# Kernel optimization log

Hardware: AMD Instinct MI355X
Metric: run time of the kernel (lower is better)

Reference implementation:

```python
import jax, jax.numpy as jnp
import numpy as np

B, C_IN, N_IN, N_OUT = 4, 64, 8192, 8192
D1, F, H = 4, 15, 16384  # d+1, filter_size, max_hash_cnt
C_MID, C_OUT = 64, 64
LEAK = 0.01


def setup_inputs() -> dict:
    key = jax.random.key(0)
    ks = jax.random.split(key, 10)
    features = jax.random.normal(ks[0], (B, C_IN, N_IN), jnp.float32)
    in_barycentric = jax.random.uniform(ks[1], (B, D1, N_IN), dtype=jnp.float32)
    # global flat lattice offsets: local vertex id in [0,H) plus per-batch base b*(H+1)
    local_off = jax.random.randint(ks[2], (B, D1, N_IN), 0, H)
    base = (jnp.arange(B, dtype=jnp.int64) * (H + 1))[:, None, None]
    in_lattice_offset = local_off.astype(jnp.int64) + base
    # neighbor ids in [-1, H); -1 means missing -> maps to zero padding slot after +1
    blur_neighbors = (jax.random.randint(ks[3], (B, F, H), 0, H + 1) - 1).astype(jnp.int64)
    out_barycentric = jax.random.uniform(ks[4], (B, D1, N_OUT), dtype=jnp.float32)
    out_lattice_offset = jax.random.randint(ks[5], (B, D1, N_OUT), 0, H).astype(jnp.int64)
    # blur conv params: layer0 Conv2d(C_IN,C_MID,(F,1)) + LeakyReLU, layer1 Conv2d(C_MID,C_OUT,(1,1)) no relu
    W0 = jax.random.normal(ks[6], (C_MID, C_IN, F), jnp.float32) * 0.05
    b0 = jax.random.normal(ks[7], (C_MID,), jnp.float32) * 0.01
    W1 = jax.random.normal(ks[8], (C_OUT, C_MID), jnp.float32) * 0.1
    b1 = jax.random.normal(ks[9], (C_OUT,), jnp.float32) * 0.01
    bias = jnp.zeros((C_OUT,), jnp.float32)  # slice bias, initialized to zeros as in module
    return dict(features=features, in_barycentric=in_barycentric,
                in_lattice_offset=in_lattice_offset, blur_neighbors=blur_neighbors,
                out_barycentric=out_barycentric, out_lattice_offset=out_lattice_offset,
                W0=W0, b0=b0, W1=W1, b1=b1, bias=bias)


def reference(features, in_barycentric, in_lattice_offset, blur_neighbors,
              out_barycentric, out_lattice_offset, W0, b0, W1, b1, bias):
    b_sz, c_in, n_in = features.shape
    max_hash = blur_neighbors.shape[-1]
    # ---- splat: scatter-sum barycentric-weighted features onto lattice vertices ----
    vals = in_barycentric[:, None, :, :] * features[:, :, None, :]      # (B,C,d1,N)
    vals = vals.transpose(0, 2, 3, 1).reshape(-1, c_in)                  # (B*d1*N, C)
    idx = (in_lattice_offset + 1).reshape(-1)                            # (B*d1*N,)
    splat = jax.ops.segment_sum(vals, idx, num_segments=b_sz * (max_hash + 1))
    splat = splat.reshape(b_sz, max_hash + 1, c_in).transpose(0, 2, 1)   # (B,C,H+1)
    # normalization: splat of all-ones feature
    one_splat = jax.ops.segment_sum(in_barycentric.reshape(-1), idx,
                                    num_segments=b_sz * (max_hash + 1))
    one_splat = one_splat.reshape(b_sz, max_hash + 1)
    splat = splat / (one_splat + 1e-5)[:, None, :]
    # ---- blur: gather F neighbors per vertex, then conv over the filter axis ----
    spread = jax.vmap(lambda s, n: s[:, n])(splat, blur_neighbors + 1)   # (B,C,F,H)
    h0 = jnp.einsum('bcfh,ocf->boh', spread, W0) + b0[None, :, None]     # (B,C_mid,H)
    h0 = jnp.where(h0 > 0, h0, LEAK * h0)                                # LeakyReLU
    feat_blurred = jnp.einsum('boh,po->bph', h0, W1) + b1[None, :, None] # (B,C_out,H)
    # ---- slice: barycentric-weighted gather back to output points ----
    tmp = jax.vmap(lambda f, o: f[:, o])(feat_blurred, out_lattice_offset)  # (B,C_out,d1,N_out)
    sliced = (out_barycentric[:, None, :, :] * tmp).sum(axis=2)
    sliced = sliced + bias[None, :, None]
    return sliced
```

## Files before the change

### kernel.cpp

```cpp
#include <hip/hip_runtime.h>

#define NB 4
#define C_IN 64
#define N_IN 8192
#define N_OUT 8192
#define D1 4
#define FS 15
#define HSZ 16384
#define LEAK 0.01f
#define CAP 24
#define POISON 0xAAAAAAAAu

#define NVERT (NB*(HSZ+1))

typedef __attribute__((ext_vector_type(8))) short short8;
typedef __attribute__((ext_vector_type(4))) float floatx4;

#define SPLATB_OFF 0
#define SPLATB_FL  (NVERT*32)
#define W0B_OFF    (SPLATB_OFF + SPLATB_FL)
#define W0B_FL     (64*64*FS/2)
#define W1B_OFF    (W0B_OFF + W0B_FL)
#define W1B_FL     (64*64/2)
#define CNT_OFF    (W1B_OFF + W1B_FL)
#define CNT_FL     (NVERT)
#define BREG_OFF   (CNT_OFF + CNT_FL)
#define FEATB_OFF  (BREG_OFF)
#define FEATB_FL   (NB*N_IN*32)
#define ENTP_OFF   (FEATB_OFF + FEATB_FL)
#define ENTP_FL    (NVERT*CAP*2)
#define FB_OFF     (BREG_OFF)

__device__ inline ushort f2bf(float x) {
    uint u = __float_as_uint(x);
    return (ushort)((u + 0x7FFF + ((u >> 16) & 1)) >> 16);
}
__device__ inline float bf2f(ushort b) {
    return __uint_as_float(((uint)b) << 16);
}

__global__ __launch_bounds__(256) void prep(const float* __restrict__ feat,
                                            const float* __restrict__ W0,
                                            const float* __restrict__ W1,
                                            const int* __restrict__ off,
                                            const float* __restrict__ bary,
                                            ushort* __restrict__ featB,
                                            ushort* __restrict__ W0f,
                                            ushort* __restrict__ W1f,
                                            uint* __restrict__ cnt,
                                            int2* __restrict__ entp) {
    __shared__ float t[64 * 65];
    const int blk = blockIdx.x;
    const int tid = threadIdx.x;
    if (blk < 512) {
        const int b  = blk >> 7;
        const int nb = (blk & 127) << 6;
        const int l  = tid & 63;
        const int g  = tid >> 6;
#pragma unroll
        for (int i = 0; i < 16; ++i) {
            int c = g * 16 + i;
            t[c * 65 + l] = feat[((size_t)(b * 64 + c)) * N_IN + nb + l];
        }
        __syncthreads();
#pragma unroll
        for (int i = 0; i < 16; ++i) {
            int n = g * 16 + i;
            featB[((size_t)(b * N_IN) + nb + n) * 64 + l] = f2bf(t[l * 65 + n]);
        }
    } else if (blk < 1024) {
        int e = (blk - 512) * 256 + tid;
        int v = off[e] + 1;
        int n = e & (N_IN - 1);
        int b = e >> 15;
        uint old  = atomicAdd(&cnt[v], 1u);
        uint slot = (old >= POISON) ? (old - POISON) : old;
        if (slot < CAP) {
            int2 pr;
            pr.x = b * N_IN + n;
            pr.y = __float_as_int(bary[e]);
            entp[v * CAP + slot] = pr;
        }
    } else {
        int e = (blk - 1024) * 256 + tid;
        if (e < 64 * 64 * FS) {
            int j    = e & 7;
            int lane = (e >> 3) & 63;
            int ch   = (e >> 9) & 1;
            int ot   = (e >> 10) & 3;
            int f    = e >> 12;
            int o = ot * 16 + (lane & 15);
            int c = ch * 32 + ((lane >> 4) & 3) * 8 + j;
            W0f[e] = f2bf(W0[(o * 64 + c) * FS + f]);
        } else {
            int e2   = e - 64 * 64 * FS;
            int j    = e2 & 7;
            int lane = (e2 >> 3) & 63;
            int ch   = (e2 >> 9) & 1;
            int pt   = (e2 >> 10) & 3;
            int p = pt * 16 + (lane & 15);
            int o = ch * 32 + ((lane >> 4) & 3) * 8 + j;
            W1f[e2] = f2bf(W1[p * 64 + o]);
        }
    }
}

__global__ __launch_bounds__(256) void gather_splat(const ushort* __restrict__ featB,
                                                    uint* __restrict__ cnt,
                                                    const int2* __restrict__ entp,
                                                    ushort* __restrict__ splatB) {
    const int v    = blockIdx.x * 4 + (threadIdx.x >> 6);
    const int lane = threadIdx.x & 63;
    const int base = v * CAP;

    uint cv = cnt[v];
    int2 p0[4];
#pragma unroll
    for (int k = 0; k < 4; ++k)
        p0[k] = entp[base + k];
    if (lane == 0) cnt[v] = 0u;

    int c = (int)((cv >= POISON) ? (cv - POISON) : cv);
    if (c > CAP) c = CAP;

    float acc = 0.f, sw = 0.f;
    {
        const int kn = c;
        float fv[4];
#pragma unroll
        for (int k = 0; k < 4; ++k)
            fv[k] = bf2f(featB[(size_t)(p0[k].x & (NB * N_IN - 1)) * 64 + lane]);
#pragma unroll
        for (int k = 0; k < 4; ++k)
            if (k < kn) {
                float w = __int_as_float(p0[k].y);
                acc += w * fv[k]; sw += w;
            }
    }
    for (int e0 = 4; e0 < c; e0 += 4) {
        const int kn = c - e0;
        int2 p[4];
#pragma unroll
        for (int k = 0; k < 4; ++k)
            p[k] = entp[base + e0 + k];
        float fv[4];
#pragma unroll
        for (int k = 0; k < 4; ++k)
            if (k < kn) fv[k] = bf2f(featB[(size_t)(p[k].x & (NB * N_IN - 1)) * 64 + lane]);
#pragma unroll
        for (int k = 0; k < 4; ++k)
            if (k < kn) {
                float w = __int_as_float(p[k].y);
                acc += w * fv[k]; sw += w;
            }
    }
    splatB[(size_t)v * 64 + lane] = f2bf(acc / (sw + 1e-5f));
}

#define XSTR 72
__global__ __launch_bounds__(256, 4) void blur_mfma(const ushort* __restrict__ splatB,
                                                    const int* __restrict__ nbr,
                                                    const ushort* __restrict__ W0f,
                                                    const ushort* __restrict__ W1f,
                                                    const float* __restrict__ b0,
                                                    const float* __restrict__ b1,
                                                    ushort* __restrict__ fb) {
    __shared__ ushort Xs[2][64 * XSTR];

    const int tid = threadIdx.x;
    const int p   = blockIdx.x;
    const int b   = p & 3;
    const int hb  = (p >> 2) << 6;

    const int lane = tid & 63;
    const int w    = tid >> 6;
    const int ow   = w & 1;
    const int hw   = w >> 1;
    const int m    = lane & 15;
    const int q    = lane >> 4;

    const int r    = tid >> 2;
    const int sseg = (tid & 3) << 4;

    const int* nbase = nbr + (b * FS) * HSZ + hb;
    const size_t sbase = (size_t)b * (HSZ + 1) * 64;

    short8 acur[2][2], anxt[2][2];
#pragma unroll
    for (int ot = 0; ot < 2; ++ot)
#pragma unroll
        for (int ch = 0; ch < 2; ++ch)
            acur[ot][ch] = *(const short8*)&W0f[(((ow * 2 + ot) * 2 + ch) * 64 + lane) * 8];

    {
        int v = nbase[r] + 1;
        const ushort* row = splatB + sbase + (size_t)v * 64 + sseg;
        *(short8*)&Xs[0][r * XSTR + sseg]     = *(const short8*)&row[0];
        *(short8*)&Xs[0][r * XSTR + sseg + 8] = *(const short8*)&row[8];
    }
    int nv = nbase[HSZ + r] + 1;
    __syncthreads();

    floatx4 acc[2][2] = {};

    for (int f = 0; f < FS; ++f) {
        const int cur = f & 1, nxt = cur ^ 1;
        short8 px0, px1;
        int nn = 0;
        if (f < FS - 1) {
            const ushort* row = splatB + sbase + (size_t)nv * 64 + sseg;
            px0 = *(const short8*)&row[0];
            px1 = *(const short8*)&row[8];
#pragma unroll
            for (int ot = 0; ot < 2; ++ot)
#pragma unroll
                for (int ch = 0; ch < 2; ++ch)
                    anxt[ot][ch] = *(const short8*)
                        &W0f[((((f + 1) * 4 + ow * 2 + ot) * 2 + ch) * 64 + lane) * 8];
            if (f < FS - 2) nn = nbase[(f + 2) * HSZ + r] + 1;
        }
#pragma unroll
        for (int ch = 0; ch < 2; ++ch) {
            const int ko = ch * 32 + q * 8;
#pragma unroll
            for (int ht = 0; ht < 2; ++ht) {
                short8 bb = *(const short8*)&Xs[cur][(hw * 32 + ht * 16 + m) * XSTR + ko];
                acc[0][ht] = __builtin_amdgcn_mfma_f32_16x16x32_bf16(acur[0][ch], bb, acc[0][ht], 0, 0, 0);
                acc[1][ht] = __builtin_amdgcn_mfma_f32_16x16x32_bf16(acur[1][ch], bb, acc[1][ht], 0, 0, 0);
            }
        }
        if (f < FS - 1) {
            *(short8*)&Xs[nxt][r * XSTR + sseg]     = px0;
            *(short8*)&Xs[nxt][r * XSTR + sseg + 8] = px1;
            nv = nn;
#pragma unroll
            for (int ot = 0; ot < 2; ++ot)
#pragma unroll
                for (int ch = 0; ch < 2; ++ch)
                    acur[ot][ch] = anxt[ot][ch];
        }
        __syncthreads();
    }

    short8 a2[2][2];
#pragma unroll
    for (int pt = 0; pt < 2; ++pt)
#pragma unroll
        for (int ch = 0; ch < 2; ++ch)
            a2[pt][ch] = *(const short8*)&W1f[(((ow * 2 + pt) * 2 + ch) * 64 + lane) * 8];

    ushort* Hs = &Xs[0][0];
#pragma unroll
    for (int ot = 0; ot < 2; ++ot) {
        const float4 b0v = *(const float4*)(b0 + ow * 32 + ot * 16 + q * 4);
#pragma unroll
        for (int ht = 0; ht < 2; ++ht) {
            float v0 = acc[ot][ht][0] + b0v.x; v0 = v0 > 0.f ? v0 : LEAK * v0;
            float v1 = acc[ot][ht][1] + b0v.y; v1 = v1 > 0.f ? v1 : LEAK * v1;
            float v2 = acc[ot][ht][2] + b0v.z; v2 = v2 > 0.f ? v2 : LEAK * v2;
            float v3 = acc[ot][ht][3] + b0v.w; v3 = v3 > 0.f ? v3 : LEAK * v3;
            ushort4 hv;
            hv.x = f2bf(v0); hv.y = f2bf(v1); hv.z = f2bf(v2); hv.w = f2bf(v3);
            *(ushort4*)&Hs[(hw * 32 + ht * 16 + m) * XSTR + ow * 32 + ot * 16 + q * 4] = hv;
        }
    }
    __syncthreads();

    floatx4 acc2[2][2] = {};
#pragma unroll
    for (int ch = 0; ch < 2; ++ch) {
        const int ko = ch * 32 + q * 8;
#pragma unroll
        for (int ht = 0; ht < 2; ++ht) {
            short8 b2 = *(const short8*)&Hs[(hw * 32 + ht * 16 + m) * XSTR + ko];
            acc2[0][ht] = __builtin_amdgcn_mfma_f32_16x16x32_bf16(a2[0][ch], b2, acc2[0][ht], 0, 0, 0);
            acc2[1][ht] = __builtin_amdgcn_mfma_f32_16x16x32_bf16(a2[1][ch], b2, acc2[1][ht], 0, 0, 0);
        }
    }

#pragma unroll
    for (int pt = 0; pt < 2; ++pt) {
        const float4 b1v = *(const float4*)(b1 + ow * 32 + pt * 16 + q * 4);
#pragma unroll
        for (int ht = 0; ht < 2; ++ht) {
            ushort4 ov;
            ov.x = f2bf(acc2[pt][ht][0] + b1v.x);
            ov.y = f2bf(acc2[pt][ht][1] + b1v.y);
            ov.z = f2bf(acc2[pt][ht][2] + b1v.z);
            ov.w = f2bf(acc2[pt][ht][3] + b1v.w);
            *(ushort4*)&fb[((size_t)(b * HSZ) + hb + hw * 32 + ht * 16 + m) * 64
                           + ow * 32 + pt * 16 + q * 4] = ov;
        }
    }
}

__global__ __launch_bounds__(256) void slice_kernel(const ushort* __restrict__ fb,
                                                    const float* __restrict__ ob,
                                                    const int* __restrict__ off,
                                                    const float* __restrict__ bias,
                                                    float* __restrict__ out) {
    __shared__ float tile[64 * 17];
    const int blk  = blockIdx.x;
    const int b    = blk & 3;
    const int nb   = (blk >> 2) << 4;
    const int lane = threadIdx.x & 63;
    const int w    = threadIdx.x >> 6;

    const float bs = bias[lane];
#pragma unroll
    for (int t = 0; t < 4; ++t) {
        int nl = w * 4 + t;
        int n  = nb + nl;
        float acc = bs;
#pragma unroll
        for (int j = 0; j < D1; ++j) {
            float wj = ob[(b * D1 + j) * N_OUT + n];
            int   oj = off[(b * D1 + j) * N_OUT + n];
            acc += wj * bf2f(fb[((size_t)b * HSZ + oj) * 64 + lane]);
        }
        tile[lane * 17 + nl] = acc;
    }
    __syncthreads();
    {
        const int p  = threadIdx.x >> 2;
        const int c4 = (threadIdx.x & 3) << 2;
        float4 v;
        v.x = tile[p * 17 + c4 + 0];
        v.y = tile[p * 17 + c4 + 1];
        v.z = tile[p * 17 + c4 + 2];
        v.w = tile[p * 17 + c4 + 3];
        *(float4*)&out[((size_t)(b * 64 + p)) * N_OUT + nb + c4] = v;
    }
}

extern "C" void kernel_launch(void* const* d_in, const int* in_sizes, int n_in,
                              void* d_out, int out_size, void* d_ws, size_t ws_size,
                              hipStream_t stream) {
    const float* features = (const float*)d_in[0];
    const float* in_bary  = (const float*)d_in[1];
    const int*   in_off   = (const int*)d_in[2];
    const int*   nbr      = (const int*)d_in[3];
    const float* out_bary = (const float*)d_in[4];
    const int*   out_off  = (const int*)d_in[5];
    const float* W0       = (const float*)d_in[6];
    const float* b0       = (const float*)d_in[7];
    const float* W1       = (const float*)d_in[8];
    const float* b1       = (const float*)d_in[9];
    const float* bias     = (const float*)d_in[10];

    float*  ws     = (float*)d_ws;
    ushort* splatB = (ushort*)(ws + SPLATB_OFF);
    ushort* W0f    = (ushort*)(ws + W0B_OFF);
    ushort* W1f    = (ushort*)(ws + W1B_OFF);
    uint*   cnt    = (uint*)(ws + CNT_OFF);
    ushort* featB  = (ushort*)(ws + FEATB_OFF);
    int2*   entp   = (int2*)(ws + ENTP_OFF);
    ushort* fb     = (ushort*)(ws + FB_OFF);


    prep<<<1280, 256, 0, stream>>>(features, W0, W1, in_off, in_bary,
                                   featB, W0f, W1f, cnt, entp);
    gather_splat<<<NVERT / 4, 256, 0, stream>>>(featB, cnt, entp, splatB);
    blur_mfma<<<NB * (HSZ / 64), 256, 0, stream>>>(splatB, nbr, W0f, W1f, b0, b1, fb);
    slice_kernel<<<NB * (N_OUT / 16), 256, 0, stream>>>(fb, out_bary, out_off, bias, (float*)d_out);
}
```

Baseline: 131.5 us.

## Load blur gather operands directly into MFMA registers, drop LDS staging

The blur kernel now has each lane gather its own neighbor rows from global memory straight into MFMA B-operand registers, instead of staging them through a double-buffered shared-memory tile. This removes the per-filter-tap LDS writes, reads and __syncthreads barriers, and shrinks shared memory to the single H tile. In exchange each row is fetched redundantly by the two output-channel warps (ow=0/1), so global and L2 gather traffic roughly doubles and more registers are needed.

```diff
diff --git a/kernel.cpp b/kernel.cpp
--- a/kernel.cpp
+++ b/kernel.cpp
@@ -165,7 +165,7 @@
                                                     const float* __restrict__ b0,
                                                     const float* __restrict__ b1,
                                                     ushort* __restrict__ fb) {
-    __shared__ ushort Xs[2][64 * XSTR];
+    __shared__ ushort Hs[64 * XSTR];
 
     const int tid = threadIdx.x;
     const int p   = blockIdx.x;
@@ -179,11 +179,12 @@
     const int m    = lane & 15;
     const int q    = lane >> 4;
 
-    const int r    = tid >> 2;
-    const int sseg = (tid & 3) << 4;
-
     const int* nbase = nbr + (b * FS) * HSZ + hb;
-    const size_t sbase = (size_t)b * (HSZ + 1) * 64;
+    const ushort* sb = splatB + (size_t)b * (HSZ + 1) * 64;
+
+    const int h0  = hw * 32 + m;
+    const int h1  = h0 + 16;
+    const int koq = q * 8;
 
     short8 acur[2][2], anxt[2][2];
 #pragma unroll
@@ -192,54 +193,62 @@
         for (int ch = 0; ch < 2; ++ch)
             acur[ot][ch] = *(const short8*)&W0f[(((ow * 2 + ot) * 2 + ch) * 64 + lane) * 8];
 
+    int iv0 = nbase[h0] + 1;
+    int iv1 = nbase[h1] + 1;
+    short8 bcur[2][2], bnxt[2][2];
     {
-        int v = nbase[r] + 1;
-        const ushort* row = splatB + sbase + (size_t)v * 64 + sseg;
-        *(short8*)&Xs[0][r * XSTR + sseg]     = *(const short8*)&row[0];
-        *(short8*)&Xs[0][r * XSTR + sseg + 8] = *(const short8*)&row[8];
-    }
-    int nv = nbase[HSZ + r] + 1;
-    __syncthreads();
+        const ushort* r0 = sb + (size_t)iv0 * 64;
+        const ushort* r1 = sb + (size_t)iv1 * 64;
+        bcur[0][0] = *(const short8*)&r0[koq];
+        bcur[1][0] = *(const short8*)&r0[32 + koq];
+        bcur[0][1] = *(const short8*)&r1[koq];
+        bcur[1][1] = *(const short8*)&r1[32 + koq];
+    }
+    int nv0 = nbase[HSZ + h0] + 1;
+    int nv1 = nbase[HSZ + h1] + 1;
 
     floatx4 acc[2][2] = {};
 
     for (int f = 0; f < FS; ++f) {
-        const int cur = f & 1, nxt = cur ^ 1;
-        short8 px0, px1;
-        int nn = 0;
+        int nn0 = 0, nn1 = 0;
         if (f < FS - 1) {
-            const ushort* row = splatB + sbase + (size_t)nv * 64 + sseg;
-            px0 = *(const short8*)&row[0];
-            px1 = *(const short8*)&row[8];
+            const ushort* r0 = sb + (size_t)nv0 * 64;
+            const ushort* r1 = sb + (size_t)nv1 * 64;
+            bnxt[0][0] = *(const short8*)&r0[koq];
+            bnxt[1][0] = *(const short8*)&r0[32 + koq];
+            bnxt[0][1] = *(const short8*)&r1[koq];
+            bnxt[1][1] = *(const short8*)&r1[32 + koq];
 #pragma unroll
             for (int ot = 0; ot < 2; ++ot)
 #pragma unroll
                 for (int ch = 0; ch < 2; ++ch)
                     anxt[ot][ch] = *(const short8*)
                         &W0f[((((f + 1) * 4 + ow * 2 + ot) * 2 + ch) * 64 + lane) * 8];
-            if (f < FS - 2) nn = nbase[(f + 2) * HSZ + r] + 1;
-        }
-#pragma unroll
-        for (int ch = 0; ch < 2; ++ch) {
-            const int ko = ch * 32 + q * 8;
+            if (f < FS - 2) {
+                nn0 = nbase[(f + 2) * HSZ + h0] + 1;
+                nn1 = nbase[(f + 2) * HSZ + h1] + 1;
+            }
+        }
+#pragma unroll
+        for (int ch = 0; ch < 2; ++ch)
 #pragma unroll
             for (int ht = 0; ht < 2; ++ht) {
-                short8 bb = *(const short8*)&Xs[cur][(hw * 32 + ht * 16 + m) * XSTR + ko];
-                acc[0][ht] = __builtin_amdgcn_mfma_f32_16x16x32_bf16(acur[0][ch], bb, acc[0][ht], 0, 0, 0);
-                acc[1][ht] = __builtin_amdgcn_mfma_f32_16x16x32_bf16(acur[1][ch], bb, acc[1][ht], 0, 0, 0);
+                acc[0][ht] = __builtin_amdgcn_mfma_f32_16x16x32_bf16(acur[0][ch], bcur[ch][ht], acc[0][ht], 0, 0, 0);
+                acc[1][ht] = __builtin_amdgcn_mfma_f32_16x16x32_bf16(acur[1][ch], bcur[ch][ht], acc[1][ht], 0, 0, 0);
             }
-        }
         if (f < FS - 1) {
-            *(short8*)&Xs[nxt][r * XSTR + sseg]     = px0;
-            *(short8*)&Xs[nxt][r * XSTR + sseg + 8] = px1;
-            nv = nn;
+#pragma unroll
+            for (int ch = 0; ch < 2; ++ch)
+#pragma unroll
+                for (int ht = 0; ht < 2; ++ht)
+                    bcur[ch][ht] = bnxt[ch][ht];
 #pragma unroll
             for (int ot = 0; ot < 2; ++ot)
 #pragma unroll
                 for (int ch = 0; ch < 2; ++ch)
                     acur[ot][ch] = anxt[ot][ch];
-        }
-        __syncthreads();
+            nv0 = nn0; nv1 = nn1;
+        }
     }
 
     short8 a2[2][2];
@@ -249,7 +258,6 @@
         for (int ch = 0; ch < 2; ++ch)
             a2[pt][ch] = *(const short8*)&W1f[(((ow * 2 + pt) * 2 + ch) * 64 + lane) * 8];
 
-    ushort* Hs = &Xs[0][0];
 #pragma unroll
     for (int ot = 0; ot < 2; ++ot) {
         const float4 b0v = *(const float4*)(b0 + ow * 32 + ot * 16 + q * 4);
```

After: 151.1 us. 1.15x slower.

## Deepen blur gather pipeline to four LDS buffers, two filter taps per barrier

Applied to the files above, without the earlier changes.

The blur kernel's LDS staging grows from a double buffer to a four-slot ring. Each loop round now gathers two neighbor rows ahead and runs the MFMAs for two filter taps, which halves the number of __syncthreads and gives the global gathers more time to complete. W0 fragments are now loaded in the same round they are used instead of being prefetched one tap ahead. In exchange, LDS per block doubles, which may reduce occupancy, and register pressure rises because two gathered rows are held at once.

```diff
diff --git a/kernel.cpp b/kernel.cpp
--- a/kernel.cpp
+++ b/kernel.cpp
@@ -165,7 +165,7 @@
                                                     const float* __restrict__ b0,
                                                     const float* __restrict__ b1,
                                                     ushort* __restrict__ fb) {
-    __shared__ ushort Xs[2][64 * XSTR];
+    __shared__ ushort Xs[4][64 * XSTR];
 
     const int tid = threadIdx.x;
     const int p   = blockIdx.x;
@@ -185,61 +185,95 @@
     const int* nbase = nbr + (b * FS) * HSZ + hb;
     const size_t sbase = (size_t)b * (HSZ + 1) * 64;
 
-    short8 acur[2][2], anxt[2][2];
-#pragma unroll
-    for (int ot = 0; ot < 2; ++ot)
-#pragma unroll
-        for (int ch = 0; ch < 2; ++ch)
-            acur[ot][ch] = *(const short8*)&W0f[(((ow * 2 + ot) * 2 + ch) * 64 + lane) * 8];
-
     {
-        int v = nbase[r] + 1;
-        const ushort* row = splatB + sbase + (size_t)v * 64 + sseg;
-        *(short8*)&Xs[0][r * XSTR + sseg]     = *(const short8*)&row[0];
-        *(short8*)&Xs[0][r * XSTR + sseg + 8] = *(const short8*)&row[8];
-    }
-    int nv = nbase[HSZ + r] + 1;
+        int v0 = nbase[r] + 1;
+        int v1 = nbase[HSZ + r] + 1;
+        const ushort* r0 = splatB + sbase + (size_t)v0 * 64 + sseg;
+        const ushort* r1 = splatB + sbase + (size_t)v1 * 64 + sseg;
+        *(short8*)&Xs[0][r * XSTR + sseg]     = *(const short8*)&r0[0];
+        *(short8*)&Xs[0][r * XSTR + sseg + 8] = *(const short8*)&r0[8];
+        *(short8*)&Xs[1][r * XSTR + sseg]     = *(const short8*)&r1[0];
+        *(short8*)&Xs[1][r * XSTR + sseg + 8] = *(const short8*)&r1[8];
+    }
+    int ivA = nbase[2 * HSZ + r] + 1;
+    int ivB = nbase[3 * HSZ + r] + 1;
     __syncthreads();
 
     floatx4 acc[2][2] = {};
 
-    for (int f = 0; f < FS; ++f) {
-        const int cur = f & 1, nxt = cur ^ 1;
-        short8 px0, px1;
-        int nn = 0;
-        if (f < FS - 1) {
-            const ushort* row = splatB + sbase + (size_t)nv * 64 + sseg;
-            px0 = *(const short8*)&row[0];
-            px1 = *(const short8*)&row[8];
+    for (int rd = 0; rd < 7; ++rd) {
+        const int f0 = 2 * rd;
+        const bool haveB = rd < 6;
+
+        short8 pxA0, pxA1, pxB0 = {}, pxB1 = {};
+        {
+            const ushort* rA = splatB + sbase + (size_t)ivA * 64 + sseg;
+            pxA0 = *(const short8*)&rA[0];
+            pxA1 = *(const short8*)&rA[8];
+        }
+        if (haveB) {
+            const ushort* rB = splatB + sbase + (size_t)ivB * 64 + sseg;
+            pxB0 = *(const short8*)&rB[0];
+            pxB1 = *(const short8*)&rB[8];
+        }
+        int nnA = 0, nnB = 0;
+        if (rd < 6) nnA = nbase[(f0 + 4) * HSZ + r] + 1;
+        if (rd < 5) nnB = nbase[(f0 + 5) * HSZ + r] + 1;
+
+        short8 af[2][2][2];
+#pragma unroll
+        for (int t = 0; t < 2; ++t)
 #pragma unroll
             for (int ot = 0; ot < 2; ++ot)
 #pragma unroll
                 for (int ch = 0; ch < 2; ++ch)
-                    anxt[ot][ch] = *(const short8*)
-                        &W0f[((((f + 1) * 4 + ow * 2 + ot) * 2 + ch) * 64 + lane) * 8];
-            if (f < FS - 2) nn = nbase[(f + 2) * HSZ + r] + 1;
-        }
+                    af[t][ot][ch] = *(const short8*)
+                        &W0f[((((f0 + t) * 4 + ow * 2 + ot) * 2 + ch) * 64 + lane) * 8];
+
+#pragma unroll
+        for (int t = 0; t < 2; ++t) {
+            const ushort* Xb = &Xs[(f0 + t) & 3][0];
+#pragma unroll
+            for (int ch = 0; ch < 2; ++ch) {
+                const int ko = ch * 32 + q * 8;
+#pragma unroll
+                for (int ht = 0; ht < 2; ++ht) {
+                    short8 bb = *(const short8*)&Xb[(hw * 32 + ht * 16 + m) * XSTR + ko];
+                    acc[0][ht] = __builtin_amdgcn_mfma_f32_16x16x32_bf16(af[t][0][ch], bb, acc[0][ht], 0, 0, 0);
+                    acc[1][ht] = __builtin_amdgcn_mfma_f32_16x16x32_bf16(af[t][1][ch], bb, acc[1][ht], 0, 0, 0);
+                }
+            }
+        }
+
+        *(short8*)&Xs[(f0 + 2) & 3][r * XSTR + sseg]     = pxA0;
+        *(short8*)&Xs[(f0 + 2) & 3][r * XSTR + sseg + 8] = pxA1;
+        if (haveB) {
+            *(short8*)&Xs[(f0 + 3) & 3][r * XSTR + sseg]     = pxB0;
+            *(short8*)&Xs[(f0 + 3) & 3][r * XSTR + sseg + 8] = pxB1;
+        }
+        ivA = nnA; ivB = nnB;
+        __syncthreads();
+    }
+
+    {
+        short8 af[2][2];
+#pragma unroll
+        for (int ot = 0; ot < 2; ++ot)
+#pragma unroll
+            for (int ch = 0; ch < 2; ++ch)
+                af[ot][ch] = *(const short8*)
+                    &W0f[(((14 * 4 + ow * 2 + ot) * 2 + ch) * 64 + lane) * 8];
+        const ushort* Xb = &Xs[2][0];
 #pragma unroll
         for (int ch = 0; ch < 2; ++ch) {
             const int ko = ch * 32 + q * 8;
 #pragma unroll
             for (int ht = 0; ht < 2; ++ht) {
-                short8 bb = *(const short8*)&Xs[cur][(hw * 32 + ht * 16 + m) * XSTR + ko];
-                acc[0][ht] = __builtin_amdgcn_mfma_f32_16x16x32_bf16(acur[0][ch], bb, acc[0][ht], 0, 0, 0);
-                acc[1][ht] = __builtin_amdgcn_mfma_f32_16x16x32_bf16(acur[1][ch], bb, acc[1][ht], 0, 0, 0);
+                short8 bb = *(const short8*)&Xb[(hw * 32 + ht * 16 + m) * XSTR + ko];
+                acc[0][ht] = __builtin_amdgcn_mfma_f32_16x16x32_bf16(af[0][ch], bb, acc[0][ht], 0, 0, 0);
+                acc[1][ht] = __builtin_amdgcn_mfma_f32_16x16x32_bf16(af[1][ch], bb, acc[1][ht], 0, 0, 0);
             }
         }
-        if (f < FS - 1) {
-            *(short8*)&Xs[nxt][r * XSTR + sseg]     = px0;
-            *(short8*)&Xs[nxt][r * XSTR + sseg + 8] = px1;
-            nv = nn;
-#pragma unroll
-            for (int ot = 0; ot < 2; ++ot)
-#pragma unroll
-                for (int ch = 0; ch < 2; ++ch)
-                    acur[ot][ch] = anxt[ot][ch];
-        }
-        __syncthreads();
     }
 
     short8 a2[2][2];
```

New measurement: 130.7 us (median of 2 runs). No clear change (-0.6%).
